# Kernel optimization log

Hardware: AMD Instinct MI355X
Metric: run time of the kernel (lower is better)

Reference implementation:

```python
import jax, jax.numpy as jnp
import numpy as np

NUM_GROUPS = 32
EPS = 1e-6


def group_norm(x, gamma, beta):
    # x: [B, C, H, W]; GroupNorm over (channels-in-group, H, W)
    B, C, H, W = x.shape
    xg = x.reshape(B, NUM_GROUPS, C // NUM_GROUPS, H, W)
    mean = xg.mean(axis=(2, 3, 4), keepdims=True)
    var = xg.var(axis=(2, 3, 4), keepdims=True)
    xn = ((xg - mean) * jax.lax.rsqrt(var + EPS)).reshape(B, C, H, W)
    return xn * gamma[None, :, None, None] + beta[None, :, None, None]


def conv1x1(x, w, b):
    # 1x1 conv == channel-mixing matmul. w: [C_out, C_in]
    return jnp.einsum('bchw,oc->bohw', x, w) + b[None, :, None, None]


def setup_inputs() -> dict:
    key = jax.random.key(0)
    ks = jax.random.split(key, 6)
    B, C, H, W = 8, 256, 64, 64
    s = 1.0 / np.sqrt(C)  # fan-in scaled weights (like Conv2d default)
    inp = {
        'x': jax.random.normal(ks[0], (B, C, H, W), jnp.float32),
        'gamma': jnp.ones((C,), jnp.float32),
        'beta': jnp.zeros((C,), jnp.float32),
        'wq': jax.random.normal(ks[1], (C, C), jnp.float32) * s,
        'bq': jnp.zeros((C,), jnp.float32),
        'wk': jax.random.normal(ks[2], (C, C), jnp.float32) * s,
        'bk': jnp.zeros((C,), jnp.float32),
        'wv': jax.random.normal(ks[3], (C, C), jnp.float32) * s,
        'bv': jnp.zeros((C,), jnp.float32),
        'wo': jax.random.normal(ks[4], (C, C), jnp.float32) * s,
        'bo': jnp.zeros((C,), jnp.float32),
    }
    return inp


def reference(x, gamma, beta, wq, bq, wk, bk, wv, bv, wo, bo):
    B, C, H, W = x.shape
    h = group_norm(x, gamma, beta)
    q = conv1x1(h, wq, bq)
    k = conv1x1(h, wk, bk)
    v = conv1x1(h, wv, bv)
    # elu + 1 feature map (nonnegative kernel features)
    q = jax.nn.elu(q) + 1.0
    k = jax.nn.elu(k) + 1.0
    N = H * W
    kf = k.reshape(B, C, N)            # [B, C, N]
    vf = v.reshape(B, C, N)            # [B, C, N]
    qf = q.reshape(B, C, N)            # [B, C, N]
    # kv = k @ v^T : [B, C, C]
    kv = jnp.einsum('bcn,bdn->bcd', kf, vf)
    # h_out[b, n, d] = sum_c q[b, c, n] * kv[b, c, d]; stored channel-first
    h_out = jnp.einsum('bcn,bcd->bdn', qf, kv).reshape(B, C, H, W)
    return x + conv1x1(h_out, wo, bo)
```

## Files before the change

kernel.cpp:

```cpp
#include <hip/hip_runtime.h>
#include <math.h>

#define C_DIM 256
#define N_DIM 4096
#define B_DIM 8

typedef __attribute__((ext_vector_type(8))) short bf16x8;
typedef __attribute__((ext_vector_type(4))) float f32x4;
typedef __attribute__((ext_vector_type(8))) unsigned short us8;
typedef __attribute__((ext_vector_type(4))) unsigned short us4;

__device__ inline unsigned short f2bf(float f) {
    unsigned int u = __float_as_uint(f);
    u += 0x7fffu + ((u >> 16) & 1u);
    return (unsigned short)(u >> 16);
}

__device__ inline void gload_lds16(const void* g, void* l) {
    __builtin_amdgcn_global_load_lds(
        (const __attribute__((address_space(1))) unsigned int*)g,
        (__attribute__((address_space(3))) unsigned int*)l, 16, 0, 0);
}

__global__ __launch_bounds__(256) void gn_stats(const float* __restrict__ x,
                                                float2* __restrict__ sums) {
    int bc = blockIdx.x;
    const float* xc = x + (size_t)bc * N_DIM;
    int t = threadIdx.x;
    float s = 0.f, q = 0.f;
    for (int i = t; i < 1024; i += 256) {
        float4 v = ((const float4*)xc)[i];
        s += v.x + v.y + v.z + v.w;
        q += v.x*v.x + v.y*v.y + v.z*v.z + v.w*v.w;
    }
    #pragma unroll
    for (int off = 32; off > 0; off >>= 1) {
        s += __shfl_down(s, off);
        q += __shfl_down(q, off);
    }
    __shared__ float red[8];
    int w = t >> 6;
    if ((t & 63) == 0) { red[w*2] = s; red[w*2+1] = q; }
    __syncthreads();
    if (t == 0) {
        float S = red[0] + red[2] + red[4] + red[6];
        float Q = red[1] + red[3] + red[5] + red[7];
        sums[bc] = make_float2(S, Q);
    }
}

__global__ __launch_bounds__(256) void gn_apply(const float* __restrict__ x,
                                                const float2* __restrict__ sums,
                                                const float* __restrict__ gamma,
                                                const float* __restrict__ beta,
                                                unsigned short* __restrict__ hT) {
    int b = blockIdx.y, n0 = blockIdx.x * 64;
    int t = threadIdx.x;
    __shared__ float scale[256], shift[256];
    __shared__ unsigned short trans[64][264];

    {
        int c = t;
        int gbase = c & ~7;
        float s = 0.f, q = 0.f;
        #pragma unroll
        for (int j = 0; j < 8; j++) {
            float2 u = sums[b*256 + gbase + j];
            s += u.x; q += u.y;
        }
        float mean = s * (1.f/32768.f);
        float var  = q * (1.f/32768.f) - mean*mean;
        float inv  = rsqrtf(var + 1e-6f);
        float gm = gamma[c] * inv;
        scale[c] = gm;
        shift[c] = beta[c] - mean * gm;
    }
    __syncthreads();

    #pragma unroll
    for (int it = 0; it < 16; it++) {
        int c  = it*16 + (t >> 4);
        int nl = (t & 15) * 4;
        float4 v = *(const float4*)(x + ((size_t)(b*C_DIM + c))*N_DIM + n0 + nl);
        float sc = scale[c], sh = shift[c];
        trans[nl+0][c] = f2bf(v.x*sc + sh);
        trans[nl+1][c] = f2bf(v.y*sc + sh);
        trans[nl+2][c] = f2bf(v.z*sc + sh);
        trans[nl+3][c] = f2bf(v.w*sc + sh);
    }
    __syncthreads();

    #pragma unroll
    for (int it = 0; it < 8; it++) {
        int nl = it*8 + (t >> 5);
        int cb = (t & 31) * 8;
        us8 vv = *(us8*)&trans[nl][cb];
        *(us8*)(hT + ((size_t)b*N_DIM + n0 + nl)*C_DIM + cb) = vv;
    }
}

__global__ __launch_bounds__(256) void wcvt(const float* __restrict__ w0, const float* __restrict__ w1,
                                            const float* __restrict__ w2, const float* __restrict__ w3,
                                            unsigned short* __restrict__ o0, unsigned short* __restrict__ o1,
                                            unsigned short* __restrict__ o2, unsigned short* __restrict__ o3) {
    const float* s; unsigned short* d;
    int which = blockIdx.y;
    if (which == 0)      { s = w0; d = o0; }
    else if (which == 1) { s = w1; d = o1; }
    else if (which == 2) { s = w2; d = o2; }
    else                 { s = w3; d = o3; }
    int idx = (blockIdx.x * 256 + threadIdx.x) * 4;
    float4 v = *(const float4*)(s + idx);
    us4 r; r[0] = f2bf(v.x); r[1] = f2bf(v.y); r[2] = f2bf(v.z); r[3] = f2bf(v.w);
    *(us4*)(d + idx) = r;
}

__global__ __launch_bounds__(256) void kvred(const float* __restrict__ src, unsigned short* __restrict__ dst) {
    int gi = (blockIdx.x * 256 + threadIdx.x) * 4;
    int b = gi >> 16, idx = gi & 65535;
    float4 a = make_float4(0.f,0.f,0.f,0.f);
    #pragma unroll
    for (int sp = 0; sp < 8; sp++) {
        float4 v = *(const float4*)(src + (((size_t)b*8 + sp) << 16) + idx);
        a.x += v.x; a.y += v.y; a.z += v.z; a.w += v.w;
    }
    us4 r; r[0] = f2bf(a.x); r[1] = f2bf(a.y); r[2] = f2bf(a.z); r[3] = f2bf(a.w);
    *(us4*)(dst + ((size_t)b << 16) + idx) = r;
}

template<int MODE>
__global__ __launch_bounds__(256) void gemm_nt(
    const unsigned short* __restrict__ A, const unsigned short* __restrict__ B,
    const float* __restrict__ bias, const float* __restrict__ resid,
    void* __restrict__ Cout,
    int M, int N, int K, int splits,
    size_t sA, size_t sB, size_t sC, size_t sR)
{
    int b  = blockIdx.z / splits;
    int sp = blockIdx.z % splits;
    int Ks = K / splits;
    int k0 = sp * Ks;

    const unsigned short* Ab = A + b * sA;
    const unsigned short* Bb = B + b * sB;

    __shared__ __align__(16) char smem_raw[36864];
    unsigned short* As = (unsigned short*)smem_raw;
    unsigned short* Bs = As + 4096;

    int t = threadIdx.x;
    int w = t >> 6, l = t & 63;
    int wm = w >> 1, wn = w & 1;
    int l15 = l & 15, quad = l >> 4;

    int m_blk = blockIdx.y * 128, n_blk = blockIdx.x * 128;

    int srow = w * 16 + (l >> 2);
    int skc  = (l & 3) * 8;

    f32x4 acc[4][4];
    #pragma unroll
    for (int i = 0; i < 4; i++)
        #pragma unroll
        for (int j = 0; j < 4; j++)
            #pragma unroll
            for (int r = 0; r < 4; r++) acc[i][j][r] = 0.f;

    const unsigned short* Asw = As + (wm*64 + l15)*32 + quad*8;
    const unsigned short* Bsw = Bs + (wn*64 + l15)*32 + quad*8;
    unsigned short* Asl = As + w*512 + l*8;
    unsigned short* Bsl = Bs + w*512 + l*8;

    for (int kt = k0; kt < k0 + Ks; kt += 32) {
        #pragma unroll
        for (int rep = 0; rep < 2; rep++) {
            gload_lds16(Ab + (size_t)(m_blk + rep*64 + srow) * K + kt + skc, Asl + rep*2048);
            gload_lds16(Bb + (size_t)(n_blk + rep*64 + srow) * K + kt + skc, Bsl + rep*2048);
        }
        __syncthreads();
        bf16x8 af[4], bfr[4];
        #pragma unroll
        for (int i = 0; i < 4; i++) af[i]  = *(const bf16x8*)(Asw + i*16*32);
        #pragma unroll
        for (int j = 0; j < 4; j++) bfr[j] = *(const bf16x8*)(Bsw + j*16*32);
        #pragma unroll
        for (int i = 0; i < 4; i++)
            #pragma unroll
            for (int j = 0; j < 4; j++)
                acc[i][j] = __builtin_amdgcn_mfma_f32_16x16x32_bf16(af[i], bfr[j], acc[i][j], 0, 0, 0);
        __syncthreads();
    }

    if (MODE == 0 || MODE == 1 || MODE == 2 || MODE == 4) {
        unsigned short* ep = (unsigned short*)smem_raw;
        int row0 = wm*64 + quad*4;
        int col0 = wn*64 + l15;
        #pragma unroll
        for (int i = 0; i < 4; i++) {
            #pragma unroll
            for (int j = 0; j < 4; j++) {
                int cl = col0 + j*16;
                #pragma unroll
                for (int r = 0; r < 4; r++) {
                    int rl = row0 + i*16 + r;
                    float val = acc[i][j][r];
                    if (MODE == 0) {
                        val += bias[n_blk + cl];
                        val = val > 0.f ? val + 1.f : __expf(val);
                    } else if (MODE == 1) {
                        val += bias[m_blk + rl];
                        val = val > 0.f ? val + 1.f : __expf(val);
                    } else if (MODE == 2) {
                        val += bias[m_blk + rl];
                    }
                    ep[rl*136 + cl] = f2bf(val);
                }
            }
        }
        __syncthreads();
        unsigned short* Cb = (unsigned short*)Cout + (size_t)b * sC;
        #pragma unroll
        for (int it = 0; it < 8; it++) {
            int row = it*16 + (t >> 4);
            int col = (t & 15) * 8;
            us8 vv = *(us8*)(ep + row*136 + col);
            *(us8*)(Cb + (size_t)(m_blk + row) * N + n_blk + col) = vv;
        }
    } else {
        float* ep32 = (float*)smem_raw;
        size_t cbase = (MODE == 3) ? ((size_t)(b*splits + sp)) * sC : (size_t)b * sC;
        float* Cb = (float*)Cout + cbase;
        #pragma unroll
        for (int h = 0; h < 2; h++) {
            if (wm == h) {
                int row0 = quad*4;
                int col0 = wn*64 + l15;
                #pragma unroll
                for (int i = 0; i < 4; i++)
                    #pragma unroll
                    for (int j = 0; j < 4; j++)
                        #pragma unroll
                        for (int r = 0; r < 4; r++)
                            ep32[(row0 + i*16 + r)*140 + col0 + j*16] = acc[i][j][r];
            }
            __syncthreads();
            #pragma unroll
            for (int it = 0; it < 8; it++) {
                int rl  = it*8 + (t >> 5);
                int row = m_blk + h*64 + rl;
                int col = (t & 31) * 4;
                f32x4 vv = *(f32x4*)(ep32 + rl*140 + col);
                if (MODE == 5) {
                    float bi = bias[row];
                    const float* rp = resid + (size_t)b*sR + (size_t)row * N + n_blk + col;
                    float4 rv = *(const float4*)rp;
                    vv[0] += bi + rv.x; vv[1] += bi + rv.y;
                    vv[2] += bi + rv.z; vv[3] += bi + rv.w;
                }
                *(f32x4*)(Cb + (size_t)row * N + n_blk + col) = vv;
            }
            __syncthreads();
        }
    }
}

extern "C" void kernel_launch(void* const* d_in, const int* in_sizes, int n_in,
                              void* d_out, int out_size, void* d_ws, size_t ws_size,
                              hipStream_t stream) {
    const float* x     = (const float*)d_in[0];
    const float* gamma = (const float*)d_in[1];
    const float* beta  = (const float*)d_in[2];
    const float* wq    = (const float*)d_in[3];
    const float* bq    = (const float*)d_in[4];
    const float* wk    = (const float*)d_in[5];
    const float* bk    = (const float*)d_in[6];
    const float* wv    = (const float*)d_in[7];
    const float* bv    = (const float*)d_in[8];
    const float* wo    = (const float*)d_in[9];
    const float* bo    = (const float*)d_in[10];
    float* out = (float*)d_out;

    const size_t TEN = (size_t)B_DIM * C_DIM * N_DIM;
    unsigned short* ws16  = (unsigned short*)d_ws;
    unsigned short* hT    = ws16;
    unsigned short* qT    = hT    + TEN;
    unsigned short* kb    = qT    + TEN;
    unsigned short* vb    = kb    + TEN;
    unsigned short* houtT = vb    + TEN;
    unsigned short* kvb   = houtT + TEN;
    unsigned short* wqb   = kvb   + 524288;
    unsigned short* wkb   = wqb   + 65536;
    unsigned short* wvb   = wkb   + 65536;
    unsigned short* wob   = wvb   + 65536;
    float2*         sums  = (float2*)(wob + 65536);
    float*          kvf   = (float*)hT;

    wcvt<<<dim3(64, 4), 256, 0, stream>>>(wq, wk, wv, wo, wqb, wkb, wvb, wob);
    gn_stats<<<dim3(B_DIM*C_DIM), 256, 0, stream>>>(x, sums);
    gn_apply<<<dim3(N_DIM/64, B_DIM), 256, 0, stream>>>(x, sums, gamma, beta, hT);

    gemm_nt<0><<<dim3(2, 32, B_DIM), 256, 0, stream>>>(hT, wqb, bq, nullptr, qT,
        4096, 256, 256, 1, 1048576, 0, 1048576, 0);
    gemm_nt<1><<<dim3(32, 2, B_DIM), 256, 0, stream>>>(wkb, hT, bk, nullptr, kb,
        256, 4096, 256, 1, 0, 1048576, 1048576, 0);
    gemm_nt<2><<<dim3(32, 2, B_DIM), 256, 0, stream>>>(wvb, hT, bv, nullptr, vb,
        256, 4096, 256, 1, 0, 1048576, 1048576, 0);
    gemm_nt<3><<<dim3(2, 2, B_DIM * 8), 256, 0, stream>>>(vb, kb, nullptr, nullptr, kvf,
        256, 256, 4096, 8, 1048576, 1048576, 65536, 0);
    kvred<<<dim3(512), 256, 0, stream>>>(kvf, kvb);
    gemm_nt<4><<<dim3(2, 32, B_DIM), 256, 0, stream>>>(qT, kvb, nullptr, nullptr, houtT,
        4096, 256, 256, 1, 1048576, 65536, 1048576, 0);
    gemm_nt<5><<<dim3(32, 2, B_DIM), 256, 0, stream>>>(wob, houtT, bo, x, out,
        256, 4096, 256, 1, 0, 1048576, 1048576, 1048576);
}
```

Baseline: 202.9 us.

## Fold output projection into kv matrix and fuse prep and QKV launches

Merges weight conversion, bias packing and group-norm statistics into one prep launch, and computes Q, K and V projections in a single launch with K and V stacked as one 512-row GEMM. It reassociates the output projection: Wo is multiplied by the per-batch kv matrix first, giving a small 256x256 matrix per batch. The final GEMM then applies that matrix directly to q, so the separate hout intermediate and its full-size GEMM are dropped. The kv split-K count rises from 8 to 16 to add parallelism, at the cost of a larger fp32 partial buffer and extra bf16 rounding of the combined matrix.

```diff
diff --git a/kernel.cpp b/kernel.cpp
--- a/kernel.cpp
+++ b/kernel.cpp
@@ -22,30 +22,53 @@
         (__attribute__((address_space(3))) unsigned int*)l, 16, 0, 0);
 }
 
-__global__ __launch_bounds__(256) void gn_stats(const float* __restrict__ x,
-                                                float2* __restrict__ sums) {
-    int bc = blockIdx.x;
-    const float* xc = x + (size_t)bc * N_DIM;
+__global__ __launch_bounds__(256) void prep_kernel(
+    const float* __restrict__ wq, const float* __restrict__ wk,
+    const float* __restrict__ wv, const float* __restrict__ wo,
+    const float* __restrict__ bk, const float* __restrict__ bv,
+    const float* __restrict__ x,
+    unsigned short* __restrict__ wqb, unsigned short* __restrict__ wkvb,
+    unsigned short* __restrict__ wob, float* __restrict__ bkv,
+    float2* __restrict__ sums)
+{
+    int z = blockIdx.x;
     int t = threadIdx.x;
-    float s = 0.f, q = 0.f;
-    for (int i = t; i < 1024; i += 256) {
-        float4 v = ((const float4*)xc)[i];
-        s += v.x + v.y + v.z + v.w;
-        q += v.x*v.x + v.y*v.y + v.z*v.z + v.w*v.w;
-    }
-    #pragma unroll
-    for (int off = 32; off > 0; off >>= 1) {
-        s += __shfl_down(s, off);
-        q += __shfl_down(q, off);
-    }
-    __shared__ float red[8];
-    int w = t >> 6;
-    if ((t & 63) == 0) { red[w*2] = s; red[w*2+1] = q; }
-    __syncthreads();
-    if (t == 0) {
-        float S = red[0] + red[2] + red[4] + red[6];
-        float Q = red[1] + red[3] + red[5] + red[7];
-        sums[bc] = make_float2(S, Q);
+    if (z < 256) {
+        const float* s; unsigned short* d;
+        int which = z >> 6;
+        if (which == 0)      { s = wq; d = wqb; }
+        else if (which == 1) { s = wk; d = wkvb; }
+        else if (which == 2) { s = wv; d = wkvb + 65536; }
+        else                 { s = wo; d = wob; }
+        int idx = (z & 63) * 1024 + t * 4;
+        float4 v = *(const float4*)(s + idx);
+        us4 r; r[0] = f2bf(v.x); r[1] = f2bf(v.y); r[2] = f2bf(v.z); r[3] = f2bf(v.w);
+        *(us4*)(d + idx) = r;
+    } else if (z == 256) {
+        bkv[t]       = bk[t];
+        bkv[t + 256] = bv[t];
+    } else {
+        int bc = z - 257;
+        const float* xc = x + (size_t)bc * N_DIM;
+        float s = 0.f, q = 0.f;
+        for (int i = t; i < 1024; i += 256) {
+            float4 v = ((const float4*)xc)[i];
+            s += v.x + v.y + v.z + v.w;
+            q += v.x*v.x + v.y*v.y + v.z*v.z + v.w*v.w;
+        }
+        #pragma unroll
+        for (int off = 32; off > 0; off >>= 1) {
+            s += __shfl_down(s, off);
+            q += __shfl_down(q, off);
+        }
+        __shared__ float red[8];
+        int w = t >> 6;
+        if ((t & 63) == 0) { red[w*2] = s; red[w*2+1] = q; }
+        __syncthreads();
+        if (t == 0) {
+            sums[bc] = make_float2(red[0]+red[2]+red[4]+red[6],
+                                   red[1]+red[3]+red[5]+red[7]);
+        }
     }
 }
 
@@ -99,29 +122,13 @@
     }
 }
 
-__global__ __launch_bounds__(256) void wcvt(const float* __restrict__ w0, const float* __restrict__ w1,
-                                            const float* __restrict__ w2, const float* __restrict__ w3,
-                                            unsigned short* __restrict__ o0, unsigned short* __restrict__ o1,
-                                            unsigned short* __restrict__ o2, unsigned short* __restrict__ o3) {
-    const float* s; unsigned short* d;
-    int which = blockIdx.y;
-    if (which == 0)      { s = w0; d = o0; }
-    else if (which == 1) { s = w1; d = o1; }
-    else if (which == 2) { s = w2; d = o2; }
-    else                 { s = w3; d = o3; }
-    int idx = (blockIdx.x * 256 + threadIdx.x) * 4;
-    float4 v = *(const float4*)(s + idx);
-    us4 r; r[0] = f2bf(v.x); r[1] = f2bf(v.y); r[2] = f2bf(v.z); r[3] = f2bf(v.w);
-    *(us4*)(d + idx) = r;
-}
-
 __global__ __launch_bounds__(256) void kvred(const float* __restrict__ src, unsigned short* __restrict__ dst) {
     int gi = (blockIdx.x * 256 + threadIdx.x) * 4;
     int b = gi >> 16, idx = gi & 65535;
     float4 a = make_float4(0.f,0.f,0.f,0.f);
     #pragma unroll
-    for (int sp = 0; sp < 8; sp++) {
-        float4 v = *(const float4*)(src + (((size_t)b*8 + sp) << 16) + idx);
+    for (int sp = 0; sp < 16; sp++) {
+        float4 v = *(const float4*)(src + (((size_t)b*16 + sp) << 16) + idx);
         a.x += v.x; a.y += v.y; a.z += v.z; a.w += v.w;
     }
     us4 r; r[0] = f2bf(a.x); r[1] = f2bf(a.y); r[2] = f2bf(a.z); r[3] = f2bf(a.w);
@@ -129,31 +136,20 @@
 }
 
 template<int MODE>
-__global__ __launch_bounds__(256) void gemm_nt(
-    const unsigned short* __restrict__ A, const unsigned short* __restrict__ B,
-    const float* __restrict__ bias, const float* __restrict__ resid,
-    void* __restrict__ Cout,
-    int M, int N, int K, int splits,
-    size_t sA, size_t sB, size_t sC, size_t sR)
+__device__ __forceinline__ void gemm_body(
+    const unsigned short* __restrict__ Ab, const unsigned short* __restrict__ Bb,
+    const float* __restrict__ bias, const float* __restrict__ residb,
+    void* __restrict__ Cb,
+    int N, int K, int k0, int Ks, int m_blk, int n_blk, bool elu,
+    char* smem)
 {
-    int b  = blockIdx.z / splits;
-    int sp = blockIdx.z % splits;
-    int Ks = K / splits;
-    int k0 = sp * Ks;
-
-    const unsigned short* Ab = A + b * sA;
-    const unsigned short* Bb = B + b * sB;
-
-    __shared__ __align__(16) char smem_raw[36864];
-    unsigned short* As = (unsigned short*)smem_raw;
+    unsigned short* As = (unsigned short*)smem;
     unsigned short* Bs = As + 4096;
 
     int t = threadIdx.x;
     int w = t >> 6, l = t & 63;
     int wm = w >> 1, wn = w & 1;
     int l15 = l & 15, quad = l >> 4;
-
-    int m_blk = blockIdx.y * 128, n_blk = blockIdx.x * 128;
 
     int srow = w * 16 + (l >> 2);
     int skc  = (l & 3) * 8;
@@ -191,8 +187,8 @@
         __syncthreads();
     }
 
-    if (MODE == 0 || MODE == 1 || MODE == 2 || MODE == 4) {
-        unsigned short* ep = (unsigned short*)smem_raw;
+    if (MODE == 0 || MODE == 1 || MODE == 4) {
+        unsigned short* ep = (unsigned short*)smem;
         int row0 = wm*64 + quad*4;
         int col0 = wn*64 + l15;
         #pragma unroll
@@ -209,27 +205,24 @@
                         val = val > 0.f ? val + 1.f : __expf(val);
                     } else if (MODE == 1) {
                         val += bias[m_blk + rl];
-                        val = val > 0.f ? val + 1.f : __expf(val);
-                    } else if (MODE == 2) {
-                        val += bias[m_blk + rl];
+                        if (elu) val = val > 0.f ? val + 1.f : __expf(val);
                     }
                     ep[rl*136 + cl] = f2bf(val);
                 }
             }
         }
         __syncthreads();
-        unsigned short* Cb = (unsigned short*)Cout + (size_t)b * sC;
+        unsigned short* Cp = (unsigned short*)Cb;
         #pragma unroll
         for (int it = 0; it < 8; it++) {
             int row = it*16 + (t >> 4);
             int col = (t & 15) * 8;
             us8 vv = *(us8*)(ep + row*136 + col);
-            *(us8*)(Cb + (size_t)(m_blk + row) * N + n_blk + col) = vv;
+            *(us8*)(Cp + (size_t)(m_blk + row) * N + n_blk + col) = vv;
         }
     } else {
-        float* ep32 = (float*)smem_raw;
-        size_t cbase = (MODE == 3) ? ((size_t)(b*splits + sp)) * sC : (size_t)b * sC;
-        float* Cb = (float*)Cout + cbase;
+        float* ep32 = (float*)smem;
+        float* Cp = (float*)Cb;
         #pragma unroll
         for (int h = 0; h < 2; h++) {
             if (wm == h) {
@@ -252,16 +245,58 @@
                 f32x4 vv = *(f32x4*)(ep32 + rl*140 + col);
                 if (MODE == 5) {
                     float bi = bias[row];
-                    const float* rp = resid + (size_t)b*sR + (size_t)row * N + n_blk + col;
-                    float4 rv = *(const float4*)rp;
+                    float4 rv = *(const float4*)(residb + (size_t)row * N + n_blk + col);
                     vv[0] += bi + rv.x; vv[1] += bi + rv.y;
                     vv[2] += bi + rv.z; vv[3] += bi + rv.w;
                 }
-                *(f32x4*)(Cb + (size_t)row * N + n_blk + col) = vv;
+                *(f32x4*)(Cp + (size_t)row * N + n_blk + col) = vv;
             }
             __syncthreads();
         }
     }
+}
+
+__global__ __launch_bounds__(256) void qkv_kernel(
+    const unsigned short* __restrict__ hT, const unsigned short* __restrict__ wqb,
+    const unsigned short* __restrict__ wkvb,
+    const float* __restrict__ bq, const float* __restrict__ bkv,
+    unsigned short* __restrict__ qT, unsigned short* __restrict__ kvbuf)
+{
+    __shared__ __align__(16) char smem[36864];
+    int z = blockIdx.x;
+    if (z < 512) {
+        int b = z >> 6, rem = z & 63;
+        int m_blk = (rem >> 1) * 128, n_blk = (rem & 1) * 128;
+        gemm_body<0>(hT + (size_t)b*1048576, wqb, bq, nullptr,
+                     qT + (size_t)b*1048576,
+                     256, 256, 0, 256, m_blk, n_blk, true, smem);
+    } else {
+        int iz = z - 512;
+        int b = iz >> 7, rem = iz & 127;
+        int m_blk = (rem >> 5) * 128, n_blk = (rem & 31) * 128;
+        gemm_body<1>(wkvb, hT + (size_t)b*1048576, bkv, nullptr,
+                     kvbuf + (size_t)b*2097152,
+                     4096, 256, 0, 256, m_blk, n_blk, m_blk < 256, smem);
+    }
+}
+
+template<int MODE>
+__global__ __launch_bounds__(256) void gemm_nt(
+    const unsigned short* __restrict__ A, const unsigned short* __restrict__ B,
+    const float* __restrict__ bias, const float* __restrict__ resid,
+    void* __restrict__ Cout,
+    int N, int K, int splits,
+    size_t sA, size_t sB, size_t sC, size_t sR, int elem4)
+{
+    __shared__ __align__(16) char smem[36864];
+    int b  = blockIdx.z / splits;
+    int sp = blockIdx.z % splits;
+    int Ks = K / splits;
+    size_t cbase = (MODE == 3) ? ((size_t)(b*splits + sp)) * sC : (size_t)b * sC;
+    void* Cb = elem4 ? (void*)((float*)Cout + cbase) : (void*)((unsigned short*)Cout + cbase);
+    gemm_body<MODE>(A + b*sA, B + b*sB, bias,
+                    resid ? resid + b*sR : nullptr, Cb,
+                    N, K, sp*Ks, Ks, blockIdx.y*128, blockIdx.x*128, false, smem);
 }
 
 extern "C" void kernel_launch(void* const* d_in, const int* in_sizes, int n_in,
@@ -284,32 +319,28 @@
     unsigned short* ws16  = (unsigned short*)d_ws;
     unsigned short* hT    = ws16;
     unsigned short* qT    = hT    + TEN;
-    unsigned short* kb    = qT    + TEN;
-    unsigned short* vb    = kb    + TEN;
-    unsigned short* houtT = vb    + TEN;
-    unsigned short* kvb   = houtT + TEN;
-    unsigned short* wqb   = kvb   + 524288;
-    unsigned short* wkb   = wqb   + 65536;
-    unsigned short* wvb   = wkb   + 65536;
-    unsigned short* wob   = wvb   + 65536;
-    float2*         sums  = (float2*)(wob + 65536);
-    float*          kvf   = (float*)hT;
-
-    wcvt<<<dim3(64, 4), 256, 0, stream>>>(wq, wk, wv, wo, wqb, wkb, wvb, wob);
-    gn_stats<<<dim3(B_DIM*C_DIM), 256, 0, stream>>>(x, sums);
+    unsigned short* kvbuf = qT    + TEN;
+    unsigned short* kvb   = kvbuf + 2*TEN;
+    unsigned short* M2b   = kvb   + 524288;
+    unsigned short* wqb   = M2b   + 524288;
+    unsigned short* wkvb  = wqb   + 65536;
+    unsigned short* wob   = wkvb  + 131072;
+    float*          bkv   = (float*)(wob + 65536);
+    float2*         sums  = (float2*)(bkv + 512);
+    float*          kvf   = (float*)(sums + 2048);
+
+    prep_kernel<<<dim3(2305), 256, 0, stream>>>(wq, wk, wv, wo, bk, bv, x,
+                                                wqb, wkvb, wob, bkv, sums);
     gn_apply<<<dim3(N_DIM/64, B_DIM), 256, 0, stream>>>(x, sums, gamma, beta, hT);
-
-    gemm_nt<0><<<dim3(2, 32, B_DIM), 256, 0, stream>>>(hT, wqb, bq, nullptr, qT,
-        4096, 256, 256, 1, 1048576, 0, 1048576, 0);
-    gemm_nt<1><<<dim3(32, 2, B_DIM), 256, 0, stream>>>(wkb, hT, bk, nullptr, kb,
-        256, 4096, 256, 1, 0, 1048576, 1048576, 0);
-    gemm_nt<2><<<dim3(32, 2, B_DIM), 256, 0, stream>>>(wvb, hT, bv, nullptr, vb,
-        256, 4096, 256, 1, 0, 1048576, 1048576, 0);
-    gemm_nt<3><<<dim3(2, 2, B_DIM * 8), 256, 0, stream>>>(vb, kb, nullptr, nullptr, kvf,
-        256, 256, 4096, 8, 1048576, 1048576, 65536, 0);
+    qkv_kernel<<<dim3(1536), 256, 0, stream>>>(hT, wqb, wkvb, bq, bkv, qT, kvbuf);
+    gemm_nt<3><<<dim3(2, 2, B_DIM*16), 256, 0, stream>>>(
+        kvbuf, kvbuf + 1048576, nullptr, nullptr, kvf,
+        256, 4096, 16, 2097152, 2097152, 65536, 0, 1);
     kvred<<<dim3(512), 256, 0, stream>>>(kvf, kvb);
-    gemm_nt<4><<<dim3(2, 32, B_DIM), 256, 0, stream>>>(qT, kvb, nullptr, nullptr, houtT,
-        4096, 256, 256, 1, 1048576, 65536, 1048576, 0);
-    gemm_nt<5><<<dim3(32, 2, B_DIM), 256, 0, stream>>>(wob, houtT, bo, x, out,
-        256, 4096, 256, 1, 0, 1048576, 1048576, 1048576);
-}
+    gemm_nt<4><<<dim3(2, 2, B_DIM), 256, 0, stream>>>(
+        wob, kvb, nullptr, nullptr, M2b,
+        256, 256, 1, 0, 65536, 65536, 0, 0);
+    gemm_nt<5><<<dim3(32, 2, B_DIM), 256, 0, stream>>>(
+        M2b, qT, bo, x, out,
+        4096, 256, 1, 65536, 1048576, 1048576, 1048576, 1);
+}
```

Result: faster. 185.5 us (-8.6%).
